# Kernel optimization log

Measured on AMD Instinct MI355X. Metric: run time of the kernel, lower is better.

## Reference

```python
import jax, jax.numpy as jnp
import numpy as np

B, N = 8192, 64
S_MIN, S_MAX = 1e-4, 1e4


def setup_inputs() -> dict:
    key = jax.random.key(0)
    a = jax.random.normal(key, (B, N, N), dtype=jnp.float32)
    # SPD input: Gram matrix + jitter, as the module assumes SPD matrices
    x = a @ jnp.swapaxes(a, -1, -2) / N + 1e-3 * jnp.eye(N, dtype=jnp.float32)
    return {"x": x}


def reference(x):
    # torch.svd -> u, s, v ; for SPD input this equals the eigendecomposition
    u, s, _ = jnp.linalg.svd(x, full_matrices=False)
    s = jnp.clip(s, S_MIN, S_MAX)
    # u @ diag(log s) @ u^T, fused: [B, n, n]
    logm = jnp.einsum('bik,bk,bjk->bij', u, jnp.log(s), u)
    # SPDVectorize: upper-triangular (incl. diagonal) entries, then flatten from dim 1
    r, c = np.triu_indices(x.shape[-1])
    out = logm[..., r, c]  # [B, n(n+1)/2]
    return out.reshape(out.shape[0], -1)
```

## Files before the change

### kernel.cpp

```cpp
#include <hip/hip_runtime.h>
#include <math.h>

#define N 64
#define TRI ((N * (N + 1)) / 2)
#define MAX_SWEEPS 20
#define TOL2 1e-10f
#define WS_PER_MAT (N * N + N)

__device__ __forceinline__ void jacobi_sweeps(float g[N]) {
    const int t = threadIdx.x & 63;
    for (int sw = 0; sw < MAX_SWEEPS; ++sw) {
        float na = 0.f;
        #pragma unroll
        for (int k = 0; k < N; ++k) na = fmaf(g[k], g[k], na);
        int bad = 0;
        for (int m = 1; m < N; ++m) {
            const int q = t ^ m;
            float pt[N];
            float d = 0.f;
            #pragma unroll
            for (int k = 0; k < N; ++k) {
                const float pv = __shfl_xor(g[k], m, 64);
                pt[k] = pv;
                d = fmaf(g[k], pv, d);
            }
            const float nb = __shfl_xor(na, m, 64);
            bad |= (d * d > TOL2 * na * nb);
            const bool lower = (t < q);
            const float nlo = lower ? na : nb;
            const float nhi = lower ? nb : na;
            float c = 1.f, s = 0.f, tt = 0.f;
            if (fabsf(d) > 1e-36f) {
                const float tau = (nhi - nlo) / (2.f * d);
                tt = copysignf(1.f / (fabsf(tau) + sqrtf(fmaf(tau, tau, 1.f))), tau);
                c = 1.f / sqrtf(fmaf(tt, tt, 1.f));
                s = tt * c;
            }
            const float se = lower ? -s : s;
            const float st = lower ? -tt : tt;
            na = fmaf(st, d, na);
            #pragma unroll
            for (int k = 0; k < N; ++k) g[k] = fmaf(se, pt[k], c * g[k]);
        }
        if (!__any(bad)) break;
    }
}

__global__ __launch_bounds__(64)
void jacobi_kernel(const float* __restrict__ X, float* __restrict__ ws) {
    const int b = blockIdx.x;
    const int t = threadIdx.x;
    const float* __restrict__ Xb = X + (size_t)b * (N * N);
    float g[N];
    #pragma unroll
    for (int k = 0; k < N; ++k) g[k] = Xb[k * N + t];
    jacobi_sweeps(g);
    float* __restrict__ wb = ws + (size_t)b * WS_PER_MAT;
    float nown = 0.f;
    #pragma unroll
    for (int k = 0; k < N; ++k) {
        wb[k * N + t] = g[k];
        nown = fmaf(g[k], g[k], nown);
    }
    float sv = sqrtf(nown);
    sv = fminf(fmaxf(sv, 1e-4f), 1e4f);
    wb[N * N + t] = logf(sv) / fmaxf(nown, 1e-12f);
}

__global__ __launch_bounds__(256)
void outer_kernel(const float* __restrict__ ws, float* __restrict__ out) {
    __shared__ float S[N][N + 1];
    __shared__ float wv[N];
    const int b = blockIdx.x;
    const int tid = threadIdx.x;
    const float* __restrict__ wb = ws + (size_t)b * WS_PER_MAT;
    for (int idx = tid; idx < N * N; idx += 256)
        S[idx >> 6][idx & 63] = wb[idx];
    if (tid < N) wv[tid] = wb[N * N + tid];
    __syncthreads();
    const int tx = tid & 15, ty = tid >> 4;
    const int i0 = ty * 4, j0 = tx * 4;
    float acc[4][4];
    #pragma unroll
    for (int r = 0; r < 4; ++r)
        #pragma unroll
        for (int c_ = 0; c_ < 4; ++c_) acc[r][c_] = 0.f;
    #pragma unroll 8
    for (int t = 0; t < N; ++t) {
        const float w = wv[t];
        float si[4], sj[4];
        #pragma unroll
        for (int r = 0; r < 4; ++r) si[r] = w * S[i0 + r][t];
        #pragma unroll
        for (int c_ = 0; c_ < 4; ++c_) sj[c_] = S[j0 + c_][t];
        #pragma unroll
        for (int r = 0; r < 4; ++r)
            #pragma unroll
            for (int c_ = 0; c_ < 4; ++c_)
                acc[r][c_] = fmaf(si[r], sj[c_], acc[r][c_]);
    }
    float* __restrict__ ob = out + (size_t)b * TRI;
    #pragma unroll
    for (int r = 0; r < 4; ++r) {
        const int i = i0 + r;
        const int st = i * (2 * N + 1 - i) / 2;
        #pragma unroll
        for (int c_ = 0; c_ < 4; ++c_) {
            const int j = j0 + c_;
            if (j >= i) ob[st + (j - i)] = acc[r][c_];
        }
    }
}

__global__ __launch_bounds__(64)
void fused_kernel(const float* __restrict__ X, float* __restrict__ out) {
    __shared__ float Gt[N][N + 1];
    __shared__ float w[N];
    const int b = blockIdx.x;
    const int t = threadIdx.x;
    const float* __restrict__ Xb = X + (size_t)b * (N * N);
    float g[N];
    #pragma unroll
    for (int k = 0; k < N; ++k) g[k] = Xb[k * N + t];
    jacobi_sweeps(g);
    float nown = 0.f;
    #pragma unroll
    for (int k = 0; k < N; ++k) {
        Gt[t][k] = g[k];
        nown = fmaf(g[k], g[k], nown);
    }
    float sv = sqrtf(nown);
    sv = fminf(fmaxf(sv, 1e-4f), 1e4f);
    w[t] = logf(sv) / fmaxf(nown, 1e-12f);
    __syncthreads();
    float wr[N];
    #pragma unroll
    for (int k = 0; k < N; ++k) wr[k] = w[k];
    float* __restrict__ ob = out + (size_t)b * TRI;
    int i = 0, base = 0;
    for (int e = t; e < TRI; e += N) {
        while (base + (N - i) <= e) { base += (N - i); ++i; }
        const int j = i + (e - base);
        float acc = 0.f;
        #pragma unroll
        for (int k = 0; k < N; ++k)
            acc = fmaf(wr[k] * Gt[k][i], Gt[k][j], acc);
        ob[e] = acc;
    }
}

extern "C" void kernel_launch(void* const* d_in, const int* in_sizes, int n_in,
                              void* d_out, int out_size, void* d_ws, size_t ws_size,
                              hipStream_t stream) {
    const float* x = (const float*)d_in[0];
    float* out = (float*)d_out;
    const int B = in_sizes[0] / (N * N);
    const size_t need = (size_t)B * WS_PER_MAT * sizeof(float);
    if (ws_size >= need) {
        jacobi_kernel<<<dim3(B), dim3(64), 0, stream>>>(x, (float*)d_ws);
        outer_kernel<<<dim3(B), dim3(256), 0, stream>>>((const float*)d_ws, out);
    } else {
        fused_kernel<<<dim3(B), dim3(64), 0, stream>>>(x, out);
    }
}
```

Baseline: 4.205 ms.

## Loosen Jacobi tolerance, split dot-product accumulators, use rsqrt, raise occupancy hint

The Jacobi convergence tolerance is loosened so fewer sweeps run before every pair counts as orthogonal. The norm and dot-product reductions now use four independent accumulators to shorten the FMA dependency chain. The cosine uses rsqrtf in place of 1/sqrtf. The jacobi kernel gets a launch_bounds minimum-blocks hint of 3, which may limit registers and cause spills given the 64-float g and pt arrays. The looser tolerance trades accuracy for speed.

```diff
diff --git a/kernel.cpp b/kernel.cpp
--- a/kernel.cpp
+++ b/kernel.cpp
@@ -4,26 +4,38 @@
 #define N 64
 #define TRI ((N * (N + 1)) / 2)
 #define MAX_SWEEPS 20
-#define TOL2 1e-10f
+#define TOL2 1e-7f
 #define WS_PER_MAT (N * N + N)
 
 __device__ __forceinline__ void jacobi_sweeps(float g[N]) {
     const int t = threadIdx.x & 63;
     for (int sw = 0; sw < MAX_SWEEPS; ++sw) {
-        float na = 0.f;
+        float n0 = 0.f, n1 = 0.f, n2 = 0.f, n3 = 0.f;
         #pragma unroll
-        for (int k = 0; k < N; ++k) na = fmaf(g[k], g[k], na);
+        for (int k = 0; k < N; k += 4) {
+            n0 = fmaf(g[k],     g[k],     n0);
+            n1 = fmaf(g[k + 1], g[k + 1], n1);
+            n2 = fmaf(g[k + 2], g[k + 2], n2);
+            n3 = fmaf(g[k + 3], g[k + 3], n3);
+        }
+        float na = (n0 + n1) + (n2 + n3);
         int bad = 0;
         for (int m = 1; m < N; ++m) {
             const int q = t ^ m;
             float pt[N];
-            float d = 0.f;
+            float d0 = 0.f, d1 = 0.f, d2 = 0.f, d3 = 0.f;
             #pragma unroll
-            for (int k = 0; k < N; ++k) {
-                const float pv = __shfl_xor(g[k], m, 64);
-                pt[k] = pv;
-                d = fmaf(g[k], pv, d);
+            for (int k = 0; k < N; k += 4) {
+                pt[k]     = __shfl_xor(g[k],     m, 64);
+                pt[k + 1] = __shfl_xor(g[k + 1], m, 64);
+                pt[k + 2] = __shfl_xor(g[k + 2], m, 64);
+                pt[k + 3] = __shfl_xor(g[k + 3], m, 64);
+                d0 = fmaf(g[k],     pt[k],     d0);
+                d1 = fmaf(g[k + 1], pt[k + 1], d1);
+                d2 = fmaf(g[k + 2], pt[k + 2], d2);
+                d3 = fmaf(g[k + 3], pt[k + 3], d3);
             }
+            const float d = (d0 + d1) + (d2 + d3);
             const float nb = __shfl_xor(na, m, 64);
             bad |= (d * d > TOL2 * na * nb);
             const bool lower = (t < q);
@@ -33,7 +45,7 @@
             if (fabsf(d) > 1e-36f) {
                 const float tau = (nhi - nlo) / (2.f * d);
                 tt = copysignf(1.f / (fabsf(tau) + sqrtf(fmaf(tau, tau, 1.f))), tau);
-                c = 1.f / sqrtf(fmaf(tt, tt, 1.f));
+                c = rsqrtf(fmaf(tt, tt, 1.f));
                 s = tt * c;
             }
             const float se = lower ? -s : s;
@@ -46,7 +58,7 @@
     }
 }
 
-__global__ __launch_bounds__(64)
+__global__ __launch_bounds__(64, 3)
 void jacobi_kernel(const float* __restrict__ X, float* __restrict__ ws) {
     const int b = blockIdx.x;
     const int t = threadIdx.x;
```

After: 4.605 ms. +9.5%, slower.
